# Performance work log

Measured on AMD Instinct MI355X. Metric: run time of the kernel, lower is better.

## Reference

```python
import jax, jax.numpy as jnp
import numpy as np

ALPHA = 0.2  # LeakyReLU negative slope
NEG_INF = -9e15


def setup_inputs() -> dict:
    key = jax.random.key(0)
    k1, k2, k3, k4 = jax.random.split(key, 4)
    B, N, Fin, Fout = 4, 4096, 256, 128
    h = jax.random.normal(k1, (B, N, Fin), dtype=jnp.float32)
    adj = jax.random.randint(k2, (B, N, N), 0, 2, dtype=jnp.int32)  # {0,1} adjacency
    # xavier_uniform with gain 1.414
    limW = 1.414 * np.sqrt(6.0 / (Fin + Fout))
    W = jax.random.uniform(k3, (Fin, Fout), jnp.float32, -limW, limW)
    lima = 1.414 * np.sqrt(6.0 / (2 * Fout + 1))
    a = jax.random.uniform(k4, (2 * Fout, 1), jnp.float32, -lima, lima)
    return {"h": h, "adj": adj, "W": W, "a": a}


def reference(h, adj, W, a):
    # Wh: [B, N, Fout]
    Wh = jnp.einsum('bni,io->bno', h, W)
    Fout = W.shape[1]
    # Decompose a^T [Wh_i || Wh_j] = a1.Wh_i + a2.Wh_j (identical math, avoids
    # materializing the [B,N,N,2F] concat tensor the torch code builds).
    a1, a2 = a[:Fout, 0], a[Fout:, 0]
    s1 = jnp.einsum('bno,o->bn', Wh, a1)  # [B, N]
    s2 = jnp.einsum('bno,o->bn', Wh, a2)  # [B, N]
    e = jax.nn.leaky_relu(s1[:, :, None] + s2[:, None, :], negative_slope=ALPHA)  # [B,N,N]
    attention = jnp.where(adj > 0, e, jnp.asarray(NEG_INF, e.dtype))
    attention = jax.nn.softmax(attention, axis=2)
    # dropout is inactive in eval mode (training=False)
    # Faithful to the torch code: the FIRST h_prime is overwritten; the output is
    # einsum('bjk,bji->bki', attention, Wh) -> sums over the softmax (row) axis j.
    h_prime = jnp.einsum('bjk,bji->bki', attention, Wh)  # [B, N, Fout]
    return jax.nn.elu(h_prime)  # concat=True
```

## Files before the change

kernel.cpp:

```cpp
#include <hip/hip_runtime.h>
#include <hip/hip_bf16.h>

#define ALPHA 0.2f
#define L2E 1.4426950408889634f

constexpr int Nn = 4096;
constexpr int FIN = 256;
constexpr int FOUT = 128;
constexpr int JC = 8;
constexpr int JQ = 512;
constexpr int NCH = 16;
constexpr long long SLAB = 2097152;

typedef __attribute__((ext_vector_type(8))) short short8;
typedef __attribute__((ext_vector_type(8))) unsigned short ushort8;
typedef __attribute__((ext_vector_type(4))) float f32x4;
typedef __attribute__((ext_vector_type(4))) int int4v;
typedef __attribute__((ext_vector_type(4))) unsigned int uint4v;

__device__ __forceinline__ unsigned short f2bf(float x) {
  unsigned int u = __float_as_uint(x);
  unsigned int r = (u + 0x7fffu + ((u >> 16) & 1u)) >> 16;
  return (unsigned short)r;
}

__device__ __forceinline__ float bf2f(unsigned short v) {
  return __uint_as_float(((unsigned)v) << 16);
}

__device__ __forceinline__ void gload16(const void* g, void* l) {
  auto lp = (__attribute__((address_space(3))) void*)l;
  auto gp = (const __attribute__((address_space(1))) void*)g;
  __builtin_amdgcn_global_load_lds(gp, lp, 16, 0, 0);
}

__global__ __launch_bounds__(256) void k0_prep(
    const float* __restrict__ W, unsigned short* __restrict__ WT) {
  __shared__ float lw[32][132];
  int t = threadIdx.x;
  int kc0 = blockIdx.x * 32;
#pragma unroll
  for (int m = 0; m < 4; ++m) {
    int idx = t * 16 + m * 4;
    f32x4 v = *(const f32x4*)(W + kc0 * 128 + idx);
    int k = idx >> 7, i0 = idx & 127;
    *(f32x4*)&lw[k][i0] = v;
  }
  __syncthreads();
  int i = t >> 1, half = t & 1;
  unsigned short pk[16];
#pragma unroll
  for (int kk = 0; kk < 16; ++kk) pk[kk] = f2bf(lw[half * 16 + kk][i]);
  ushort8* dst = (ushort8*)(WT + i * 256 + kc0 + half * 16);
  dst[0] = *(ushort8*)&pk[0];
  dst[1] = *(ushort8*)&pk[8];
}

__global__ __launch_bounds__(256) void k1b_wh(
    const float* __restrict__ h, const unsigned short* __restrict__ WT,
    const float* __restrict__ a, unsigned short* __restrict__ whT,
    float* __restrict__ s1L, float* __restrict__ s2L) {
  __shared__ __align__(16) char smem[36864];
  int t = threadIdx.x;
  int w = t >> 6, l = t & 63, g = l >> 4, r = l & 15;
  int r0 = blockIdx.x * 16;
  int b = r0 >> 12, nbase = r0 & 4095;

  f32x4 acc[2];
  acc[0] = (f32x4){0.f, 0.f, 0.f, 0.f};
  acc[1] = (f32x4){0.f, 0.f, 0.f, 0.f};

  for (int kc = 0; kc < 2; ++kc) {
    __syncthreads();
    {
      int row = t >> 4, sec = t & 15;
      const f32x4* src =
          (const f32x4*)(h + (long long)(r0 + row) * 256 + kc * 128 + sec * 8);
      f32x4 v0 = src[0], v1 = src[1];
      unsigned int pk[4];
      pk[0] = ((unsigned)f2bf(v0.y) << 16) | f2bf(v0.x);
      pk[1] = ((unsigned)f2bf(v0.w) << 16) | f2bf(v0.z);
      pk[2] = ((unsigned)f2bf(v1.y) << 16) | f2bf(v1.x);
      pk[3] = ((unsigned)f2bf(v1.w) << 16) | f2bf(v1.z);
      *(ushort8*)(smem + row * 256 + ((sec ^ (row & 7)) << 4)) = *(ushort8*)pk;
    }
    {
      int i = t >> 1, pt = t & 1;
      const ushort8* src = (const ushort8*)(WT + i * 256 + kc * 128 + pt * 64);
#pragma unroll
      for (int m = 0; m < 8; ++m) {
        ushort8 v = src[m];
        int slot = pt * 8 + m;
        *(ushort8*)(smem + 4096 + i * 256 + ((slot ^ (i & 7)) << 4)) = v;
      }
    }
    __syncthreads();
#pragma unroll
    for (int kk = 0; kk < 4; ++kk) {
      short8 af =
          *(const short8*)(smem + r * 256 + (((kk * 4 + g) ^ (r & 7)) << 4));
#pragma unroll
      for (int s = 0; s < 2; ++s) {
        int i = w * 32 + s * 16 + r;
        short8 bf = *(const short8*)(smem + 4096 + i * 256 +
                                     (((kk * 4 + g) ^ (i & 7)) << 4));
        acc[s] =
            __builtin_amdgcn_mfma_f32_16x16x32_bf16(af, bf, acc[s], 0, 0, 0);
      }
    }
  }

  __syncthreads();
  unsigned short* tb = (unsigned short*)smem;
#pragma unroll
  for (int s = 0; s < 2; ++s)
#pragma unroll
    for (int q = 0; q < 4; ++q)
      tb[(w * 32 + s * 16 + r) * 25 + g * 4 + q] = f2bf(acc[s][q]);
  __syncthreads();

  {
    int i = t >> 1, half = t & 1;
    ushort8 v = *(const ushort8*)(tb + i * 25 + half * 8);
    *(ushort8*)(whT + (((long long)(b * 128 + i)) << 12) + nbase + half * 8) =
        v;
  }
  {
    int n = t >> 4, seg = t & 15;
    f32x4 a10 = *(const f32x4*)(a + seg * 8);
    f32x4 a11 = *(const f32x4*)(a + seg * 8 + 4);
    f32x4 a20 = *(const f32x4*)(a + 128 + seg * 8);
    f32x4 a21 = *(const f32x4*)(a + 128 + seg * 8 + 4);
    float v1 = 0.f, v2 = 0.f;
#pragma unroll
    for (int m = 0; m < 8; ++m) {
      float wh = bf2f(tb[(seg * 8 + m) * 25 + n]);
      float c1 = (m < 4) ? a10[m] : a11[m - 4];
      float c2 = (m < 4) ? a20[m] : a21[m - 4];
      v1 += wh * c1;
      v2 += wh * c2;
    }
#pragma unroll
    for (int off = 8; off; off >>= 1) {
      v1 += __shfl_xor(v1, off);
      v2 += __shfl_xor(v2, off);
    }
    if (seg == 0) {
      s1L[r0 + n] = v1 * L2E;
      s2L[r0 + n] = v2 * L2E;
    }
  }
}

__global__ __launch_bounds__(256) void k2_stats(
    const int* __restrict__ adj, const float* __restrict__ s1L,
    const float* __restrict__ s2L, float2* __restrict__ st2,
    unsigned long long* __restrict__ mask64) {
  __shared__ unsigned int mwords[128];
  __shared__ float wsum[4];
  int row = blockIdx.x;
  int b = row >> 12;
  int t = threadIdx.x;
  float s1j = s1L[row];
  const int4v* arow = (const int4v*)(adj + (long long)row * Nn);
  const f32x4* s2v = (const f32x4*)(s2L + (b << 12));

  float sum = 0.f;
#pragma unroll
  for (int q = 0; q < 4; ++q) {
    int4v av = __builtin_nontemporal_load(arow + q * 256 + t);
    f32x4 sv = s2v[q * 256 + t];
    unsigned nib = 0;
#pragma unroll
    for (int c = 0; c < 4; ++c) {
      float u = s1j + sv[c];
      float vL = fmaxf(u, ALPHA * u);
      float e = exp2f(vL);
      sum = fmaf((float)av[c], e, sum);
      nib |= ((unsigned)av[c]) << c;
    }
    unsigned n1 = nib | (__shfl_xor(nib, 1) << 4);
    unsigned n2 = n1 | (__shfl_xor(n1, 2) << 8);
    unsigned n4 = n2 | (__shfl_xor(n2, 4) << 16);
    if ((t & 7) == 0) mwords[q * 32 + (t >> 3)] = n4;
  }
#pragma unroll
  for (int off = 32; off; off >>= 1) sum += __shfl_xor(sum, off);
  if ((t & 63) == 0) wsum[t >> 6] = sum;
  __syncthreads();
  if (t < 64) {
    unsigned long long mv = *(unsigned long long*)&mwords[t * 2];
    mask64[((long long)row << 6) + t] = mv;
  }
  if (t == 0) {
    float S = wsum[0] + wsum[1] + wsum[2] + wsum[3];
    float negc = (S > 0.f) ? -log2f(S) : -1.0e30f;
    st2[row] =
        make_float2(exp2f(s1j + negc), exp2f(ALPHA * s1j + negc));
  }
}

__global__ __launch_bounds__(512, 6) void k3_pv(
    const unsigned short* __restrict__ whT, const float2* __restrict__ st2,
    const unsigned long long* __restrict__ mask64,
    const float* __restrict__ s2L, unsigned short* __restrict__ pbuf) {
  __shared__ __align__(16) char smem[28672];
  unsigned int* mkpl = (unsigned int*)(smem + 16384);
  float2* stl = (float2*)(smem + 24576);

  int t = threadIdx.x;
  int orig = blockIdx.x;
  int x = orig & 7, mm = orig >> 3;
  int b = x >> 1;
  int kt = ((x & 1) << 4) | (mm & 15);
  int jc = mm >> 4;
  int w = t >> 6, l = t & 63;
  int lh = l >> 4;
  int lo = l & 15;
  int ks = w;
  int jq0 = jc * JQ;
  long long brow = (long long)(b << 12);
  int k0g = kt << 7;
  float z1 = s2L[brow + k0g + ks * 16 + lo];
  float F1 = exp2f(z1);
  float F2 = exp2f(ALPHA * z1);
  int sh31 = 31 - (((ks & 1) << 4) + lo);
  int wsel = ks >> 1;

  if (t < 256) gload16(st2 + brow + jq0 + t * 2, (char*)stl + t * 16);
  {
    uint4v mrow = *(const uint4v*)((const char*)(mask64 +
                                                 ((brow + jq0 + t) << 6)) +
                                   kt * 16);
    mkpl[0 * 512 + t] = mrow[0];
    mkpl[1 * 512 + t] = mrow[1];
    mkpl[2 * 512 + t] = mrow[2];
    mkpl[3 * 512 + t] = mrow[3];
  }
  const unsigned short* whTb = whT + ((long long)b << 19);
  int gi = t & 127;
  const unsigned short* wsrc0 =
      whTb + (long long)gi * 4096 + jq0 + (t >> 7) * 8;
  gload16(wsrc0, smem + t * 16);
  __syncthreads();

  f32x4 acc[8];
#pragma unroll
  for (int q = 0; q < 8; ++q) acc[q] = (f32x4){0.f, 0.f, 0.f, 0.f};

  const unsigned int* mkw = mkpl + wsel * 512;
  for (int ch = 0; ch < NCH; ++ch) {
    int cur = ch & 1;
    if (ch + 1 < NCH)
      gload16(wsrc0 + (ch + 1) * 32, smem + (cur ^ 1) * 8192 + t * 16);
    char* wb = smem + cur * 8192;
    int jb = ch * 32 + lh * 8;
    uint4v mw0 = *(const uint4v*)(mkw + jb);
    uint4v mw1 = *(const uint4v*)(mkw + jb + 4);
    const f32x4* stp = (const f32x4*)(stl + jb);
    f32x4 sA = stp[0], sB = stp[1], sC = stp[2], sD = stp[3];
    short8 af;
#pragma unroll
    for (int e = 0; e < 8; ++e) {
      f32x4 sv = (e < 2) ? sA : (e < 4) ? sB : (e < 6) ? sC : sD;
      float E1 = (e & 1) ? sv.z : sv.x;
      float E2 = (e & 1) ? sv.w : sv.y;
      unsigned mv = (e < 4) ? mw0[e] : mw1[e - 4];
      float p = fmaxf(E1 * F1, E2 * F2);
      int msk = ((int)(mv << sh31)) >> 31;
      unsigned pu = __float_as_uint(p) & (unsigned)msk;
      __hip_bfloat16 hb = __float2bfloat16(__uint_as_float(pu));
      af[e] = *(short*)&hb;
    }
#pragma unroll
    for (int q = 0; q < 8; ++q) {
      short8 bv = *(const short8*)(wb + ((lh * 128 + q * 16 + lo) << 4));
      acc[q] = __builtin_amdgcn_mfma_f32_16x16x32_bf16(af, bv, acc[q], 0, 0, 0);
    }
    __syncthreads();
  }

  unsigned short* pb = pbuf + (long long)jc * SLAB + ((brow + k0g) << 7);
#pragma unroll
  for (int q = 0; q < 8; ++q) {
#pragma unroll
    for (int r = 0; r < 4; ++r) {
      int kl = ks * 16 + lh * 4 + r;
      pb[kl * 128 + q * 16 + lo] = f2bf(acc[q][r]);
    }
  }
}

__global__ __launch_bounds__(256) void k4_reduce(
    const unsigned short* __restrict__ pbuf, float* __restrict__ out) {
  int orig = blockIdx.x;
  int n = (orig & 7) * 128 + (orig >> 3);
  int base = (n * 256 + threadIdx.x) * 8;
  float s[8] = {0.f, 0.f, 0.f, 0.f, 0.f, 0.f, 0.f, 0.f};
#pragma unroll
  for (int sl = 0; sl < JC; ++sl) {
    ushort8 v = *(const ushort8*)(pbuf + (long long)sl * SLAB + base);
#pragma unroll
    for (int e = 0; e < 8; ++e)
      s[e] += __uint_as_float(((unsigned)(unsigned short)v[e]) << 16);
  }
  f32x4 o0, o1;
#pragma unroll
  for (int e = 0; e < 8; ++e) {
    float xv = s[e];
    float y = xv > 0.f ? xv : expm1f(xv);
    if (e < 4) o0[e] = y; else o1[e - 4] = y;
  }
  *(f32x4*)(out + base) = o0;
  *(f32x4*)(out + base + 4) = o1;
}

extern "C" void kernel_launch(void* const* d_in, const int* in_sizes, int n_in,
                              void* d_out, int out_size, void* d_ws,
                              size_t ws_size, hipStream_t stream) {
  const float* h = (const float*)d_in[0];
  const int* adj = (const int*)d_in[1];
  const float* W = (const float*)d_in[2];
  const float* a = (const float*)d_in[3];
  float* out = (float*)d_out;

  char* ws = (char*)d_ws;
  unsigned short* WT = (unsigned short*)ws;
  unsigned short* whT = (unsigned short*)(ws + (1 << 20));
  float* s1L = (float*)(ws + (5 << 20));
  float* s2L = s1L + 16384;
  float2* st2 = (float2*)(ws + (5 << 20) + (128 << 10));
  unsigned long long* mask64 =
      (unsigned long long*)(ws + (6 << 20));
  unsigned short* pbuf = (unsigned short*)(ws + (16 << 20));

  hipLaunchKernelGGL(k0_prep, dim3(8), dim3(256), 0, stream, W, WT);
  hipLaunchKernelGGL(k1b_wh, dim3(1024), dim3(256), 0, stream, h, WT, a, whT,
                     s1L, s2L);
  hipLaunchKernelGGL(k2_stats, dim3(16384), dim3(256), 0, stream, adj, s1L,
                     s2L, st2, mask64);
  hipLaunchKernelGGL(k3_pv, dim3(1024), dim3(512), 0, stream, whT, st2,
                     mask64, s2L, pbuf);
  hipLaunchKernelGGL(k4_reduce, dim3(1024), dim3(256), 0, stream, pbuf, out);
}
```

Before: 109.5 us.

## Double k-tile per wave in PV kernel to reuse Wh B-fragments

Each wave in k3_pv now handles two 16-column k sub-tiles (256 k per block instead of 128), computing two masked probability fragments and issuing two MFMAs per loaded Wh fragment. The block count halves to 512, mask staging doubles, and LDS grows slightly. This aims to halve the Wh shared-memory and global loads per unit of MFMA work. The cost is more accumulator registers (launch bounds lowered to 4 waves/EU), fewer blocks for latency hiding, and a switch of the final store rounding to the intrinsic bf16 conversion.

```diff
diff --git a/kernel.cpp b/kernel.cpp
--- a/kernel.cpp
+++ b/kernel.cpp
@@ -200,42 +200,48 @@
   }
 }
 
-__global__ __launch_bounds__(512, 6) void k3_pv(
+__global__ __launch_bounds__(512, 4) void k3_pv(
     const unsigned short* __restrict__ whT, const float2* __restrict__ st2,
     const unsigned long long* __restrict__ mask64,
     const float* __restrict__ s2L, unsigned short* __restrict__ pbuf) {
-  __shared__ __align__(16) char smem[28672];
+  __shared__ __align__(16) char smem[36864];
   unsigned int* mkpl = (unsigned int*)(smem + 16384);
-  float2* stl = (float2*)(smem + 24576);
+  float2* stl = (float2*)(smem + 32768);
 
   int t = threadIdx.x;
   int orig = blockIdx.x;
   int x = orig & 7, mm = orig >> 3;
   int b = x >> 1;
-  int kt = ((x & 1) << 4) | (mm & 15);
-  int jc = mm >> 4;
+  int kt = ((x & 1) << 3) | (mm & 7);
+  int jc = mm >> 3;
   int w = t >> 6, l = t & 63;
   int lh = l >> 4;
   int lo = l & 15;
   int ks = w;
   int jq0 = jc * JQ;
   long long brow = (long long)(b << 12);
-  int k0g = kt << 7;
-  float z1 = s2L[brow + k0g + ks * 16 + lo];
-  float F1 = exp2f(z1);
-  float F2 = exp2f(ALPHA * z1);
-  int sh31 = 31 - (((ks & 1) << 4) + lo);
-  int wsel = ks >> 1;
+  int k0g = kt << 8;
+  float z1a = s2L[brow + k0g + ks * 32 + lo];
+  float z1b = s2L[brow + k0g + ks * 32 + 16 + lo];
+  float F1a = exp2f(z1a), F2a = exp2f(ALPHA * z1a);
+  float F1b = exp2f(z1b), F2b = exp2f(ALPHA * z1b);
+  int shA = 31 - lo;
+  int shB = 15 - lo;
 
   if (t < 256) gload16(st2 + brow + jq0 + t * 2, (char*)stl + t * 16);
   {
-    uint4v mrow = *(const uint4v*)((const char*)(mask64 +
-                                                 ((brow + jq0 + t) << 6)) +
-                                   kt * 16);
-    mkpl[0 * 512 + t] = mrow[0];
-    mkpl[1 * 512 + t] = mrow[1];
-    mkpl[2 * 512 + t] = mrow[2];
-    mkpl[3 * 512 + t] = mrow[3];
+    const char* msrc =
+        (const char*)(mask64 + ((brow + jq0 + t) << 6)) + kt * 32;
+    uint4v m0 = *(const uint4v*)msrc;
+    uint4v m1 = *(const uint4v*)(msrc + 16);
+    mkpl[0 * 512 + t] = m0[0];
+    mkpl[1 * 512 + t] = m0[1];
+    mkpl[2 * 512 + t] = m0[2];
+    mkpl[3 * 512 + t] = m0[3];
+    mkpl[4 * 512 + t] = m1[0];
+    mkpl[5 * 512 + t] = m1[1];
+    mkpl[6 * 512 + t] = m1[2];
+    mkpl[7 * 512 + t] = m1[3];
   }
   const unsigned short* whTb = whT + ((long long)b << 19);
   int gi = t & 127;
@@ -244,11 +250,15 @@
   gload16(wsrc0, smem + t * 16);
   __syncthreads();
 
-  f32x4 acc[8];
-#pragma unroll
-  for (int q = 0; q < 8; ++q) acc[q] = (f32x4){0.f, 0.f, 0.f, 0.f};
-
-  const unsigned int* mkw = mkpl + wsel * 512;
+  f32x4 accA[8], accB[8];
+#pragma unroll
+  for (int q = 0; q < 8; ++q) {
+    accA[q] = (f32x4){0.f, 0.f, 0.f, 0.f};
+    accB[q] = (f32x4){0.f, 0.f, 0.f, 0.f};
+  }
+
+  const unsigned int* mkw = mkpl + ks * 512;
+#pragma unroll 1
   for (int ch = 0; ch < NCH; ++ch) {
     int cur = ch & 1;
     if (ch + 1 < NCH)
@@ -259,23 +269,31 @@
     uint4v mw1 = *(const uint4v*)(mkw + jb + 4);
     const f32x4* stp = (const f32x4*)(stl + jb);
     f32x4 sA = stp[0], sB = stp[1], sC = stp[2], sD = stp[3];
-    short8 af;
+    short8 afA, afB;
 #pragma unroll
     for (int e = 0; e < 8; ++e) {
       f32x4 sv = (e < 2) ? sA : (e < 4) ? sB : (e < 6) ? sC : sD;
       float E1 = (e & 1) ? sv.z : sv.x;
       float E2 = (e & 1) ? sv.w : sv.y;
       unsigned mv = (e < 4) ? mw0[e] : mw1[e - 4];
-      float p = fmaxf(E1 * F1, E2 * F2);
-      int msk = ((int)(mv << sh31)) >> 31;
-      unsigned pu = __float_as_uint(p) & (unsigned)msk;
-      __hip_bfloat16 hb = __float2bfloat16(__uint_as_float(pu));
-      af[e] = *(short*)&hb;
+      float pA = fmaxf(E1 * F1a, E2 * F2a);
+      float pB = fmaxf(E1 * F1b, E2 * F2b);
+      int mA = ((int)(mv << shA)) >> 31;
+      int mB = ((int)(mv << shB)) >> 31;
+      unsigned puA = __float_as_uint(pA) & (unsigned)mA;
+      unsigned puB = __float_as_uint(pB) & (unsigned)mB;
+      __hip_bfloat16 hA = __float2bfloat16(__uint_as_float(puA));
+      __hip_bfloat16 hB = __float2bfloat16(__uint_as_float(puB));
+      afA[e] = *(short*)&hA;
+      afB[e] = *(short*)&hB;
     }
 #pragma unroll
     for (int q = 0; q < 8; ++q) {
       short8 bv = *(const short8*)(wb + ((lh * 128 + q * 16 + lo) << 4));
-      acc[q] = __builtin_amdgcn_mfma_f32_16x16x32_bf16(af, bv, acc[q], 0, 0, 0);
+      accA[q] =
+          __builtin_amdgcn_mfma_f32_16x16x32_bf16(afA, bv, accA[q], 0, 0, 0);
+      accB[q] =
+          __builtin_amdgcn_mfma_f32_16x16x32_bf16(afB, bv, accB[q], 0, 0, 0);
     }
     __syncthreads();
   }
@@ -285,8 +303,12 @@
   for (int q = 0; q < 8; ++q) {
 #pragma unroll
     for (int r = 0; r < 4; ++r) {
-      int kl = ks * 16 + lh * 4 + r;
-      pb[kl * 128 + q * 16 + lo] = f2bf(acc[q][r]);
+      int klA = ks * 32 + lh * 4 + r;
+      int klB = klA + 16;
+      __hip_bfloat16 hA = __float2bfloat16(accA[q][r]);
+      __hip_bfloat16 hB = __float2bfloat16(accB[q][r]);
+      pb[klA * 128 + q * 16 + lo] = *(unsigned short*)&hA;
+      pb[klB * 128 + q * 16 + lo] = *(unsigned short*)&hB;
     }
   }
 }
@@ -339,7 +361,7 @@
                      s1L, s2L);
   hipLaunchKernelGGL(k2_stats, dim3(16384), dim3(256), 0, stream, adj, s1L,
                      s2L, st2, mask64);
-  hipLaunchKernelGGL(k3_pv, dim3(1024), dim3(512), 0, stream, whT, st2,
+  hipLaunchKernelGGL(k3_pv, dim3(512), dim3(512), 0, stream, whT, st2,
                      mask64, s2L, pbuf);
   hipLaunchKernelGGL(k4_reduce, dim3(1024), dim3(256), 0, stream, pbuf, out);
 }
```

New measurement: 106.8 us. 2.4% less time.
